# Kernel tuning notes

Measured on AMD Instinct MI355X. Metric: run time of the kernel, lower is better.

The kernel has to match this reference:

```python
import jax, jax.numpy as jnp
import numpy as np

N = 100000
E = 1600000
ROUND = 2


def spmm(src, dst, x):
    # adj.matmul(x) with binary sparse adjacency given as edge list:
    # out[dst] += x[src]
    return jax.ops.segment_sum(x[src], dst, num_segments=N)


def setup_inputs() -> dict:
    key = jax.random.key(0)
    ks = jax.random.split(key, 8)
    x = jax.random.normal(ks[0], (N, 512), dtype=jnp.float32)
    W_embed = jax.random.normal(ks[1], (512, 64), dtype=jnp.float32) * (1.0 / np.sqrt(512))
    b_embed = jnp.zeros((64,), dtype=jnp.float32)
    W_cls = jax.random.normal(ks[2], (448, 40), dtype=jnp.float32) * (1.0 / np.sqrt(448))
    b_cls = jnp.zeros((40,), dtype=jnp.float32)
    adj_src = jax.random.randint(ks[3], (E,), 0, N, dtype=jnp.int32)
    adj_dst = jax.random.randint(ks[4], (E,), 0, N, dtype=jnp.int32)
    adj2_src = jax.random.randint(ks[5], (E,), 0, N, dtype=jnp.int32)
    adj2_dst = jax.random.randint(ks[6], (E,), 0, N, dtype=jnp.int32)
    return {"x": x, "W_embed": W_embed, "b_embed": b_embed, "W_cls": W_cls,
            "b_cls": b_cls, "adj_src": adj_src, "adj_dst": adj_dst,
            "adj2_src": adj2_src, "adj2_dst": adj2_dst}


def reference(x, W_embed, b_embed, W_cls, b_cls, adj_src, adj_dst, adj2_src, adj2_dst):
    # embed: Linear + ReLU
    h = jax.nn.relu(x @ W_embed + b_embed)  # [N, 64]
    hidden_reps = [h]
    for _ in range(ROUND):
        r1 = spmm(adj_src, adj_dst, h)      # 1-hop aggregation
        r2 = spmm(adj2_src, adj2_dst, h)    # 2-hop aggregation
        h = jnp.concatenate([r1, r2], axis=-1)
        hidden_reps.append(h)
    hf = jnp.concatenate(hidden_reps, axis=-1)  # [N, 64*(2^(ROUND+1)-1)] = [N, 448]
    # dropout is identity in eval mode
    logits = hf @ W_cls + b_cls
    return jax.nn.log_softmax(logits, axis=1)
```

## Files before the change

### kernel.cpp

```cpp
#include <hip/hip_runtime.h>
#include <hip/hip_bf16.h>

#define NN 100000
#define EE 1600000
#define NBK 196
#define BSH 9
#define EPB 4096
#define NBA 391
#define STG 10240
#define CAP 9216

using frag8 = __attribute__((ext_vector_type(8))) short;
using f32x4 = __attribute__((ext_vector_type(4))) float;

__device__ inline unsigned short f2bf(float f) {
    unsigned u = __float_as_uint(f);
    u = u + 0x7FFFu + ((u >> 16) & 1u);
    return (unsigned short)(u >> 16);
}
__device__ inline unsigned pack_bf16(float a, float b) {
    __hip_bfloat162 h = __float22bfloat162_rn(float2{a, b});
    union { __hip_bfloat162 h2; unsigned u; } c;
    c.h2 = h;
    return c.u;
}
__device__ inline unsigned char f2fp8(float v) {
    unsigned p = __builtin_amdgcn_cvt_pk_fp8_f32(v, v, 0, false);
    return (unsigned char)(p & 0xff);
}


__global__ __launch_bounds__(256) void prep1_k(const int* __restrict__ s1,
                                               const int* __restrict__ d1,
                                               const int* __restrict__ s2,
                                               const int* __restrict__ d2,
                                               int* __restrict__ bcur,
                                               unsigned* __restrict__ tmp1,
                                               unsigned* __restrict__ tmp2,
                                               const float* __restrict__ W,
                                               unsigned short* __restrict__ Wbf,
                                               const float* __restrict__ Wc,
                                               unsigned short* __restrict__ Wbig) {
    __shared__ int lhist[NBK], lbase[NBK], gbase[NBK], lcur[NBK];
    __shared__ int sscan[256];
    __shared__ int stot;
    __shared__ uint2 stage[EPB];
    int blk = blockIdx.x;
    int t = threadIdx.x;

    if (blk >= 2 * NBA) {
        int wb = blk - 2 * NBA;
        if (wb < 128) {
            int id = wb * 256 + t;
            if (id < 512 * 64) {
                int k = id >> 6, col = id & 63;
                int ch = k >> 3, el = k & 7;
                int cs = (ch & ~15) | ((ch & 15) ^ (col & 7));
                Wbf[col * 512 + cs * 8 + el] = f2bf(W[id]);
            }
        } else {
            int id = (wb - 128) * 256 + t;
            int k = id >> 7, col = id & 127;
            float v = 0.f;
            if (col < 40) v = Wc[k * 40 + col];
            else if (col < 80)  { if (k >= 64) v = Wc[(192 + k - 64) * 40 + (col - 40)]; }
            else if (col < 120) { if (k >= 64) v = Wc[(320 + k - 64) * 40 + (col - 80)]; }
            int ch = k >> 3, el = k & 7;
            int phys = (ch & ~7) | ((ch & 7) ^ (col & 7));
            Wbig[col * 192 + phys * 8 + el] = f2bf(v);
        }
        return;
    }

    int adj = blk / NBA;
    int chunk = blk % NBA;
    const int* ss = adj ? s2 : s1;
    const int* dd = adj ? d2 : d1;
    unsigned* tmp = adj ? tmp2 : tmp1;
    for (int i = t; i < NBK; i += 256) { lhist[i] = 0; lcur[i] = 0; }
    __syncthreads();
    int e0 = chunk * EPB;
    int d[16], s[16];
    #pragma unroll
    for (int k = 0; k < 16; ++k) {
        int e = e0 + k * 256 + t;
        d[k] = (e < EE) ? dd[e] : -1;
        s[k] = (e < EE) ? ss[e] : 0;
        if (d[k] >= 0) atomicAdd(&lhist[d[k] >> BSH], 1);
    }
    __syncthreads();
    int hv = (t < NBK) ? lhist[t] : 0;
    sscan[t] = hv;
    __syncthreads();
    for (int off = 1; off < 256; off <<= 1) {
        int u = (t >= off) ? sscan[t - off] : 0;
        __syncthreads();
        sscan[t] += u;
        __syncthreads();
    }
    if (t < NBK) lbase[t] = sscan[t] - hv;
    if (t == NBK - 1) stot = sscan[t];
    __syncthreads();
    for (int i = t; i < NBK; i += 256)
        gbase[i] = lhist[i] ? atomicAdd(&bcur[adj * NBK + i], lhist[i]) : 0;
    __syncthreads();
    #pragma unroll
    for (int k = 0; k < 16; ++k) {
        if (d[k] >= 0) {
            int b = d[k] >> BSH;
            int pos = lbase[b] + atomicAdd(&lcur[b], 1);
            stage[pos] = make_uint2((unsigned)d[k], (unsigned)s[k]);
        }
    }
    __syncthreads();
    int tot = stot;
    for (int i = t; i < tot; i += 256) {
        uint2 u = stage[i];
        int b = u.x >> BSH;
        int off = gbase[b] + (i - lbase[b]);
        if (off < CAP)
            tmp[(size_t)b * CAP + off] = ((u.x & 511u) << 17) | u.y;
    }
}


__global__ __launch_bounds__(256) void binB_k(const unsigned* __restrict__ tmp1,
                                              const unsigned* __restrict__ tmp2,
                                              const int* __restrict__ bcur,
                                              int2* __restrict__ rse1,
                                              int2* __restrict__ rse2,
                                              int* __restrict__ csr1,
                                              int* __restrict__ csr2) {
    __shared__ int cnt[512], cur[512];
    __shared__ int sscan[256];
    __shared__ int stage[STG];
    int adj = blockIdx.y, b = blockIdx.x;
    const unsigned* tmp = adj ? tmp2 : tmp1;
    int2* rse = adj ? rse2 : rse1;
    int* csr  = adj ? csr2 : csr1;
    int t = threadIdx.x;
    int n0 = b << BSH;
    int n1 = n0 + 512; if (n1 > NN) n1 = NN;
    int nn = n1 - n0;
    int base = b * CAP;
    int count = bcur[adj * NBK + b];
    if (count > CAP) count = CAP;
    cnt[t] = 0; cnt[t + 256] = 0;
    __syncthreads();
    for (int i = t; i < count; i += 256)
        atomicAdd(&cnt[tmp[base + i] >> 17], 1);
    __syncthreads();
    int c0 = cnt[2 * t], c1 = cnt[2 * t + 1];
    int ps = c0 + c1;
    sscan[t] = ps;
    __syncthreads();
    for (int off = 1; off < 256; off <<= 1) {
        int u = (t >= off) ? sscan[t - off] : 0;
        __syncthreads();
        sscan[t] += u;
        __syncthreads();
    }
    int pe = sscan[t] - ps;
    int e0x = pe, e1x = pe + c0;
    if (2 * t < nn)     rse[n0 + 2 * t]     = make_int2(base + e0x, c0);
    if (2 * t + 1 < nn) rse[n0 + 2 * t + 1] = make_int2(base + e1x, c1);
    cur[2 * t] = e0x; cur[2 * t + 1] = e1x;
    __syncthreads();
    for (int i = t; i < count; i += 256) {
        unsigned u = tmp[base + i];
        int loc = atomicAdd(&cur[u >> 17], 1);
        int src = (int)(u & 0x1FFFFu);
        if (loc < STG) stage[loc] = src;
        else csr[base + loc] = src;
    }
    __syncthreads();
    int m = count < STG ? count : STG;
    for (int i = t; i < m; i += 256) csr[base + i] = stage[i];
}


__global__ __launch_bounds__(256) void embed_k(const float* __restrict__ x,
                                               const unsigned short* __restrict__ Wbf,
                                               const float* __restrict__ bias,
                                               unsigned short* __restrict__ hcat,
                                               unsigned char* __restrict__ h0f8) {
    __shared__ unsigned short sW[64 * 128];
    int tid = threadIdx.x;
    int lane = tid & 63, wave = tid >> 6;
    int row0 = blockIdx.x * 64;
    f32x4 acc[4];
    #pragma unroll
    for (int n = 0; n < 4; n++) acc[n] = (f32x4){0.f, 0.f, 0.f, 0.f};

    int arow = row0 + wave * 16 + (lane & 15);
    bool valid = arow < NN;
    const float* xrow = x + (size_t)(valid ? arow : 0) * 512 + (lane >> 4) * 8;

    for (int kt = 0; kt < 4; ++kt) {
        for (int q = tid; q < 1024; q += 256) {
            int col = q >> 4, c = q & 15;
            ((uint4*)sW)[q] = ((const uint4*)Wbf)[col * 64 + kt * 16 + c];
        }
        __syncthreads();
        #pragma unroll
        for (int kk = 0; kk < 4; ++kk) {
            const float4* px = (const float4*)(xrow + kt * 128 + kk * 32);
            float4 p0 = px[0], p1 = px[1];
            frag8 a;
            unsigned* au = (unsigned*)&a;
            if (valid) {
                au[0] = pack_bf16(p0.x, p0.y);
                au[1] = pack_bf16(p0.z, p0.w);
                au[2] = pack_bf16(p1.x, p1.y);
                au[3] = pack_bf16(p1.z, p1.w);
            } else {
                au[0] = 0; au[1] = 0; au[2] = 0; au[3] = 0;
            }
            #pragma unroll
            for (int n = 0; n < 4; n++) {
                int col = n * 16 + (lane & 15);
                int bc = (kk * 4 + (lane >> 4)) ^ (col & 7);
                frag8 b = *(const frag8*)&sW[(col * 16 + bc) * 8];
                acc[n] = __builtin_amdgcn_mfma_f32_16x16x32_bf16(a, b, acc[n], 0, 0, 0);
            }
        }
        __syncthreads();
    }
    #pragma unroll
    for (int n = 0; n < 4; n++) {
        int col = n * 16 + (lane & 15);
        float bv = bias[col];
        #pragma unroll
        for (int i = 0; i < 4; i++) {
            int r = row0 + wave * 16 + (lane >> 4) * 4 + i;
            if (r < NN) {
                float vv = acc[n][i] + bv;
                vv = vv > 0.f ? vv : 0.f;
                hcat[(size_t)r * 192 + col] = f2bf(vv);
                h0f8[(size_t)r * 64 + col] = f2fp8(vv);
            }
        }
    }
}


__device__ inline void gacc8f8(float* a, uint2 u) {
    a[0] += __builtin_amdgcn_cvt_f32_fp8(u.x, 0);
    a[1] += __builtin_amdgcn_cvt_f32_fp8(u.x, 1);
    a[2] += __builtin_amdgcn_cvt_f32_fp8(u.x, 2);
    a[3] += __builtin_amdgcn_cvt_f32_fp8(u.x, 3);
    a[4] += __builtin_amdgcn_cvt_f32_fp8(u.y, 0);
    a[5] += __builtin_amdgcn_cvt_f32_fp8(u.y, 1);
    a[6] += __builtin_amdgcn_cvt_f32_fp8(u.y, 2);
    a[7] += __builtin_amdgcn_cvt_f32_fp8(u.y, 3);
}


__global__ __launch_bounds__(256) void round1_k(const unsigned char* __restrict__ h8,
                                                unsigned short* __restrict__ hc,
                                                const int2* __restrict__ rse1,
                                                const int* __restrict__ csr1,
                                                const int2* __restrict__ rse2,
                                                const int* __restrict__ csr2) {
    int wave = threadIdx.x >> 6, lane = threadIdx.x & 63;
    int row = blockIdx.x * 4 + wave;
    int g = lane >> 3, gl = lane & 7;

    int2 v1r = rse1[row], v2r = rse2[row];
    int s1 = v1r.x, c1 = v1r.y, e1 = s1 + c1;
    int s2 = v2r.x, c2 = v2r.y, e2 = s2 + c2;
    int idx1 = 0, idx2 = 0;
    if (lane < c1) idx1 = csr1[s1 + lane];
    if (lane < c2) idx2 = csr2[s2 + lane];
    int cnt1 = c1 < 64 ? c1 : 64, cnt2 = c2 < 64 ? c2 : 64;

    float a1[8] = {0.f, 0.f, 0.f, 0.f, 0.f, 0.f, 0.f, 0.f};
    float a2[8] = {0.f, 0.f, 0.f, 0.f, 0.f, 0.f, 0.f, 0.f};

    {
        int j0 = g, j1 = 8 + g;
        int x10 = __shfl(idx1, j0), x11 = __shfl(idx1, j1);
        int x20 = __shfl(idx2, j0), x21 = __shfl(idx2, j1);
        uint2 u10 = *((const uint2*)(h8 + (size_t)x10 * 64) + gl);
        uint2 u11 = *((const uint2*)(h8 + (size_t)x11 * 64) + gl);
        uint2 u20 = *((const uint2*)(h8 + (size_t)x20 * 64) + gl);
        uint2 u21 = *((const uint2*)(h8 + (size_t)x21 * 64) + gl);
        if (j0 < cnt1) gacc8f8(a1, u10);
        if (j1 < cnt1) gacc8f8(a1, u11);
        if (j0 < cnt2) gacc8f8(a2, u20);
        if (j1 < cnt2) gacc8f8(a2, u21);
    }
    int nq1 = (cnt1 + 7) >> 3, nq2 = (cnt2 + 7) >> 3;
    int nq = nq1 > nq2 ? nq1 : nq2;
    for (int q = 2; q < nq; ++q) {
        int j = q * 8 + g;
        int y1 = __shfl(idx1, j), y2 = __shfl(idx2, j);
        uint2 w1 = *((const uint2*)(h8 + (size_t)y1 * 64) + gl);
        uint2 w2 = *((const uint2*)(h8 + (size_t)y2 * 64) + gl);
        if (j < cnt1) gacc8f8(a1, w1);
        if (j < cnt2) gacc8f8(a2, w2);
    }
    for (int t0 = s1 + 64; t0 < e1; t0 += 64) {
        int rem = e1 - t0;
        int idxv = 0;
        if (lane < rem) idxv = csr1[t0 + lane];
        int cnt = rem < 64 ? rem : 64;
        int nqt = (cnt + 7) >> 3;
        for (int q = 0; q < nqt; ++q) {
            int j = q * 8 + g;
            int s0 = __shfl(idxv, j);
            uint2 u = *((const uint2*)(h8 + (size_t)s0 * 64) + gl);
            if (j < cnt) gacc8f8(a1, u);
        }
    }
    for (int t0 = s2 + 64; t0 < e2; t0 += 64) {
        int rem = e2 - t0;
        int idxv = 0;
        if (lane < rem) idxv = csr2[t0 + lane];
        int cnt = rem < 64 ? rem : 64;
        int nqt = (cnt + 7) >> 3;
        for (int q = 0; q < nqt; ++q) {
            int j = q * 8 + g;
            int s0 = __shfl(idxv, j);
            uint2 u = *((const uint2*)(h8 + (size_t)s0 * 64) + gl);
            if (j < cnt) gacc8f8(a2, u);
        }
    }

    #pragma unroll
    for (int i = 0; i < 8; ++i) {
        a1[i] += __shfl_xor(a1[i], 8);
        a1[i] += __shfl_xor(a1[i], 16);
        a1[i] += __shfl_xor(a1[i], 32);
        a2[i] += __shfl_xor(a2[i], 8);
        a2[i] += __shfl_xor(a2[i], 16);
        a2[i] += __shfl_xor(a2[i], 32);
    }
    if (lane < 8) {
        uint4 o;
        o.x = pack_bf16(a1[0], a1[1]);
        o.y = pack_bf16(a1[2], a1[3]);
        o.z = pack_bf16(a1[4], a1[5]);
        o.w = pack_bf16(a1[6], a1[7]);
        *(uint4*)(hc + (size_t)row * 192 + 64 + lane * 8) = o;
    } else if (lane < 16) {
        int l = lane - 8;
        uint4 o;
        o.x = pack_bf16(a2[0], a2[1]);
        o.y = pack_bf16(a2[2], a2[3]);
        o.z = pack_bf16(a2[4], a2[5]);
        o.w = pack_bf16(a2[6], a2[7]);
        *(uint4*)(hc + (size_t)row * 192 + 128 + l * 8) = o;
    }
}


__global__ __launch_bounds__(256) void gemm_k(const unsigned short* __restrict__ hcat,
                                              const unsigned short* __restrict__ Wbig,
                                              const float* __restrict__ bc,
                                              float* __restrict__ logits,
                                              unsigned char* __restrict__ zf8) {
    __shared__ unsigned short sA[64 * 64];
    __shared__ unsigned short sB[128 * 64];
    int tid = threadIdx.x;
    int lane = tid & 63, wave = tid >> 6;
    int row0 = blockIdx.x * 64;
    f32x4 acc[8];
    #pragma unroll
    for (int n = 0; n < 8; n++) acc[n] = (f32x4){0.f, 0.f, 0.f, 0.f};

    for (int kt = 0; kt < 3; ++kt) {
        #pragma unroll
        for (int q = tid; q < 512; q += 256) {
            int r = q >> 3, c = q & 7;
            int phys = c ^ (r & 7);
            ((uint4*)sA)[r * 8 + phys] = ((const uint4*)hcat)[(size_t)(row0 + r) * 24 + kt * 8 + c];
        }
        #pragma unroll
        for (int q = tid; q < 1024; q += 256) {
            int col = q >> 3, c = q & 7;
            ((uint4*)sB)[q] = ((const uint4*)Wbig)[col * 24 + kt * 8 + c];
        }
        __syncthreads();
        #pragma unroll
        for (int kk = 0; kk < 2; ++kk) {
            int ar = wave * 16 + (lane & 15);
            int ac = (kk * 4 + (lane >> 4)) ^ (ar & 7);
            frag8 a = *(const frag8*)&sA[(ar * 8 + ac) * 8];
            #pragma unroll
            for (int n = 0; n < 8; n++) {
                int col = n * 16 + (lane & 15);
                int bcc = (kk * 4 + (lane >> 4)) ^ (col & 7);
                frag8 b = *(const frag8*)&sB[(col * 8 + bcc) * 8];
                acc[n] = __builtin_amdgcn_mfma_f32_16x16x32_bf16(a, b, acc[n], 0, 0, 0);
            }
        }
        __syncthreads();
    }
    #pragma unroll
    for (int n = 0; n < 8; n++) {
        int col = n * 16 + (lane & 15);
        float bv = (col < 40) ? bc[col] : 0.f;
        #pragma unroll
        for (int i = 0; i < 4; i++) {
            int r = row0 + wave * 16 + (lane >> 4) * 4 + i;
            if (r < NN) {
                float vv = acc[n][i];
                if (col < 40) {
                    logits[(size_t)r * 40 + col] = vv + bv;
                } else if (col < 80) {
                    zf8[(size_t)r * 128 + (col - 40)] = f2fp8(vv);
                } else if (col < 120) {
                    zf8[(size_t)r * 128 + 64 + (col - 80)] = f2fp8(vv);
                }
            }
        }
    }
}


__global__ __launch_bounds__(256) void round2_k(const unsigned char* __restrict__ z8,
                                                const int2* __restrict__ rse1,
                                                const int* __restrict__ csr1,
                                                const int2* __restrict__ rse2,
                                                const int* __restrict__ csr2,
                                                float* __restrict__ logits) {
    int wave = threadIdx.x >> 6, lane = threadIdx.x & 63;
    int row = blockIdx.x * 4 + wave;
    int g = lane >> 3, gl = lane & 7;

    int2 v1r = rse1[row], v2r = rse2[row];
    int s1 = v1r.x, c1 = v1r.y, e1 = s1 + c1;
    int s2 = v2r.x, c2 = v2r.y, e2 = s2 + c2;
    int idx1 = 0, idx2 = 0;
    if (lane < c1) idx1 = csr1[s1 + lane];
    if (lane < c2) idx2 = csr2[s2 + lane];
    int cnt1 = c1 < 64 ? c1 : 64, cnt2 = c2 < 64 ? c2 : 64;

    float a[8] = {0.f, 0.f, 0.f, 0.f, 0.f, 0.f, 0.f, 0.f};

    {
        int j0 = g, j1 = 8 + g;
        int x10 = __shfl(idx1, j0), x11 = __shfl(idx1, j1);
        int x20 = __shfl(idx2, j0), x21 = __shfl(idx2, j1);
        uint2 u10 = *((const uint2*)(z8 + (size_t)x10 * 128) + gl);
        uint2 u11 = *((const uint2*)(z8 + (size_t)x11 * 128) + gl);
        uint2 u20 = *((const uint2*)(z8 + (size_t)x20 * 128 + 64) + gl);
        uint2 u21 = *((const uint2*)(z8 + (size_t)x21 * 128 + 64) + gl);
        if (j0 < cnt1) gacc8f8(a, u10);
        if (j1 < cnt1) gacc8f8(a, u11);
        if (j0 < cnt2) gacc8f8(a, u20);
        if (j1 < cnt2) gacc8f8(a, u21);
    }
    int nq1 = (cnt1 + 7) >> 3, nq2 = (cnt2 + 7) >> 3;
    int nq = nq1 > nq2 ? nq1 : nq2;
    for (int q = 2; q < nq; ++q) {
        int j = q * 8 + g;
        int y1 = __shfl(idx1, j), y2 = __shfl(idx2, j);
        uint2 w1 = *((const uint2*)(z8 + (size_t)y1 * 128) + gl);
        uint2 w2 = *((const uint2*)(z8 + (size_t)y2 * 128 + 64) + gl);
        if (j < cnt1) gacc8f8(a, w1);
        if (j < cnt2) gacc8f8(a, w2);
    }
    for (int t0 = s1 + 64; t0 < e1; t0 += 64) {
        int rem = e1 - t0;
        int idxv = 0;
        if (lane < rem) idxv = csr1[t0 + lane];
        int cnt = rem < 64 ? rem : 64;
        int nqt = (cnt + 7) >> 3;
        for (int q = 0; q < nqt; ++q) {
            int j = q * 8 + g;
            int s0 = __shfl(idxv, j);
            uint2 u = *((const uint2*)(z8 + (size_t)s0 * 128) + gl);
            if (j < cnt) gacc8f8(a, u);
        }
    }
    for (int t0 = s2 + 64; t0 < e2; t0 += 64) {
        int rem = e2 - t0;
        int idxv = 0;
        if (lane < rem) idxv = csr2[t0 + lane];
        int cnt = rem < 64 ? rem : 64;
        int nqt = (cnt + 7) >> 3;
        for (int q = 0; q < nqt; ++q) {
            int j = q * 8 + g;
            int s0 = __shfl(idxv, j);
            uint2 u = *((const uint2*)(z8 + (size_t)s0 * 128 + 64) + gl);
            if (j < cnt) gacc8f8(a, u);
        }
    }

    #pragma unroll
    for (int i = 0; i < 8; ++i) {
        a[i] += __shfl_xor(a[i], 8);
        a[i] += __shfl_xor(a[i], 16);
        a[i] += __shfl_xor(a[i], 32);
    }

    bool act = lane < 5;
    float v[8];
    if (act) {
        float4 b0 = *(const float4*)(logits + (size_t)row * 40 + lane * 8);
        float4 b1 = *(const float4*)(logits + (size_t)row * 40 + lane * 8 + 4);
        v[0] = b0.x + a[0]; v[1] = b0.y + a[1]; v[2] = b0.z + a[2]; v[3] = b0.w + a[3];
        v[4] = b1.x + a[4]; v[5] = b1.y + a[5]; v[6] = b1.z + a[6]; v[7] = b1.w + a[7];
    } else {
        #pragma unroll
        for (int i = 0; i < 8; ++i) v[i] = -1e30f;
    }
    float m = fmaxf(fmaxf(fmaxf(v[0], v[1]), fmaxf(v[2], v[3])),
                    fmaxf(fmaxf(v[4], v[5]), fmaxf(v[6], v[7])));
    m = fmaxf(m, __shfl_xor(m, 1));
    m = fmaxf(m, __shfl_xor(m, 2));
    m = fmaxf(m, __shfl_xor(m, 4));
    float es = 0.f;
    if (act) {
        #pragma unroll
        for (int i = 0; i < 8; ++i) es += __expf(v[i] - m);
    }
    es += __shfl_xor(es, 1);
    es += __shfl_xor(es, 2);
    es += __shfl_xor(es, 4);
    float ls = __logf(es);
    if (act) {
        float4 o0, o1;
        o0.x = v[0] - m - ls; o0.y = v[1] - m - ls; o0.z = v[2] - m - ls; o0.w = v[3] - m - ls;
        o1.x = v[4] - m - ls; o1.y = v[5] - m - ls; o1.z = v[6] - m - ls; o1.w = v[7] - m - ls;
        *(float4*)(logits + (size_t)row * 40 + lane * 8)     = o0;
        *(float4*)(logits + (size_t)row * 40 + lane * 8 + 4) = o1;
    }
}


extern "C" void kernel_launch(void* const* d_in, const int* in_sizes, int n_in,
                              void* d_out, int out_size, void* d_ws, size_t ws_size,
                              hipStream_t stream) {
    const float* x       = (const float*)d_in[0];
    const float* W_embed = (const float*)d_in[1];
    const float* b_embed = (const float*)d_in[2];
    const float* W_cls   = (const float*)d_in[3];
    const float* b_cls   = (const float*)d_in[4];
    const int* a1src = (const int*)d_in[5];
    const int* a1dst = (const int*)d_in[6];
    const int* a2src = (const int*)d_in[7];
    const int* a2dst = (const int*)d_in[8];

    float* logits = (float*)d_out;
    float* ws = (float*)d_ws;

    const size_t OFF_HCAT = 0;
    const size_t OFF_H0F8 = 9600000;
    const size_t OFF_ZF8  = 11200000;
    const size_t OFF_RSE1 = 14400000;
    const size_t OFF_RSE2 = 14600000;
    const size_t OFF_BC   = 14800000;
    const size_t OFF_CSR1 = 14800392;
    const size_t OFF_CSR2 = 16606728;
    const size_t OFF_TMP1 = 18413064;
    const size_t OFF_TMP2 = 20219400;
    const size_t OFF_WBF  = 22025736;
    const size_t OFF_WBIG = 22042120;

    unsigned short* hcat = (unsigned short*)(ws + OFF_HCAT);
    unsigned char*  h0f8 = (unsigned char*)(ws + OFF_H0F8);
    unsigned char*  zf8  = (unsigned char*)(ws + OFF_ZF8);
    int2* rse1 = (int2*)(ws + OFF_RSE1);
    int2* rse2 = (int2*)(ws + OFF_RSE2);
    int*  bcur = (int*)(ws + OFF_BC);
    int*  csr1 = (int*)(ws + OFF_CSR1);
    int*  csr2 = (int*)(ws + OFF_CSR2);
    unsigned* tmp1 = (unsigned*)(ws + OFF_TMP1);
    unsigned* tmp2 = (unsigned*)(ws + OFF_TMP2);
    unsigned short* wbf  = (unsigned short*)(ws + OFF_WBF);
    unsigned short* wbig = (unsigned short*)(ws + OFF_WBIG);

    hipMemsetAsync(ws + OFF_BC, 0, 392 * 4, stream);

    prep1_k<<<2 * NBA + 224, 256, 0, stream>>>(a1src, a1dst, a2src, a2dst, bcur, tmp1, tmp2,
                                               W_embed, wbf, W_cls, wbig);
    binB_k<<<dim3(NBK, 2), 256, 0, stream>>>(tmp1, tmp2, bcur, rse1, rse2, csr1, csr2);

    embed_k<<<(NN + 63) / 64, 256, 0, stream>>>(x, wbf, b_embed, hcat, h0f8);

    round1_k<<<NN / 4, 256, 0, stream>>>(h0f8, hcat, rse1, csr1, rse2, csr2);
    gemm_k<<<(NN + 63) / 64, 256, 0, stream>>>(hcat, wbig, b_cls, logits, zf8);
    round2_k<<<NN / 4, 256, 0, stream>>>(zf8, rse1, csr1, rse2, csr2, logits);
}
```

Baseline: 251.0 us.

## Fuse CSR binning and embed GEMM into one heterogeneous kernel launch

After: 249.6 us. Within noise of the previous version (-0.6%).

```diff
diff --git a/kernel.cpp b/kernel.cpp
--- a/kernel.cpp
+++ b/kernel.cpp
@@ -7,7 +7,7 @@
 #define BSH 9
 #define EPB 4096
 #define NBA 391
-#define STG 10240
+#define STG 8704
 #define CAP 9216
 
 using frag8 = __attribute__((ext_vector_type(8))) short;
@@ -124,70 +124,74 @@
 }
 
 
-__global__ __launch_bounds__(256) void binB_k(const unsigned* __restrict__ tmp1,
-                                              const unsigned* __restrict__ tmp2,
-                                              const int* __restrict__ bcur,
-                                              int2* __restrict__ rse1,
-                                              int2* __restrict__ rse2,
-                                              int* __restrict__ csr1,
-                                              int* __restrict__ csr2) {
-    __shared__ int cnt[512], cur[512];
-    __shared__ int sscan[256];
-    __shared__ int stage[STG];
-    int adj = blockIdx.y, b = blockIdx.x;
-    const unsigned* tmp = adj ? tmp2 : tmp1;
-    int2* rse = adj ? rse2 : rse1;
-    int* csr  = adj ? csr2 : csr1;
-    int t = threadIdx.x;
-    int n0 = b << BSH;
-    int n1 = n0 + 512; if (n1 > NN) n1 = NN;
-    int nn = n1 - n0;
-    int base = b * CAP;
-    int count = bcur[adj * NBK + b];
-    if (count > CAP) count = CAP;
-    cnt[t] = 0; cnt[t + 256] = 0;
-    __syncthreads();
-    for (int i = t; i < count; i += 256)
-        atomicAdd(&cnt[tmp[base + i] >> 17], 1);
-    __syncthreads();
-    int c0 = cnt[2 * t], c1 = cnt[2 * t + 1];
-    int ps = c0 + c1;
-    sscan[t] = ps;
-    __syncthreads();
-    for (int off = 1; off < 256; off <<= 1) {
-        int u = (t >= off) ? sscan[t - off] : 0;
-        __syncthreads();
-        sscan[t] += u;
-        __syncthreads();
-    }
-    int pe = sscan[t] - ps;
-    int e0x = pe, e1x = pe + c0;
-    if (2 * t < nn)     rse[n0 + 2 * t]     = make_int2(base + e0x, c0);
-    if (2 * t + 1 < nn) rse[n0 + 2 * t + 1] = make_int2(base + e1x, c1);
-    cur[2 * t] = e0x; cur[2 * t + 1] = e1x;
-    __syncthreads();
-    for (int i = t; i < count; i += 256) {
-        unsigned u = tmp[base + i];
-        int loc = atomicAdd(&cur[u >> 17], 1);
-        int src = (int)(u & 0x1FFFFu);
-        if (loc < STG) stage[loc] = src;
-        else csr[base + loc] = src;
-    }
-    __syncthreads();
-    int m = count < STG ? count : STG;
-    for (int i = t; i < m; i += 256) csr[base + i] = stage[i];
-}
-
-
-__global__ __launch_bounds__(256) void embed_k(const float* __restrict__ x,
+__global__ __launch_bounds__(256) void prep2_k(const unsigned* __restrict__ tmp1,
+                                               const unsigned* __restrict__ tmp2,
+                                               const int* __restrict__ bcur,
+                                               int2* __restrict__ rse1,
+                                               int2* __restrict__ rse2,
+                                               int* __restrict__ csr1,
+                                               int* __restrict__ csr2,
+                                               const float* __restrict__ x,
                                                const unsigned short* __restrict__ Wbf,
                                                const float* __restrict__ bias,
                                                unsigned short* __restrict__ hcat,
                                                unsigned char* __restrict__ h0f8) {
-    __shared__ unsigned short sW[64 * 128];
-    int tid = threadIdx.x;
-    int lane = tid & 63, wave = tid >> 6;
-    int row0 = blockIdx.x * 64;
+    __shared__ __align__(16) unsigned char smem[(512 + 512 + 256 + STG) * 4];
+    int blk = blockIdx.x;
+    int t = threadIdx.x;
+
+    if (blk < 2 * NBK) {
+        int* cnt   = (int*)smem;
+        int* cur   = cnt + 512;
+        int* sscan = cur + 512;
+        int* stage = sscan + 256;
+        int adj = blk / NBK, b = blk % NBK;
+        const unsigned* tmp = adj ? tmp2 : tmp1;
+        int2* rse = adj ? rse2 : rse1;
+        int* csr  = adj ? csr2 : csr1;
+        int n0 = b << BSH;
+        int n1 = n0 + 512; if (n1 > NN) n1 = NN;
+        int nn = n1 - n0;
+        int base = b * CAP;
+        int count = bcur[adj * NBK + b];
+        if (count > CAP) count = CAP;
+        cnt[t] = 0; cnt[t + 256] = 0;
+        __syncthreads();
+        for (int i = t; i < count; i += 256)
+            atomicAdd(&cnt[tmp[base + i] >> 17], 1);
+        __syncthreads();
+        int c0 = cnt[2 * t], c1 = cnt[2 * t + 1];
+        int ps = c0 + c1;
+        sscan[t] = ps;
+        __syncthreads();
+        for (int off = 1; off < 256; off <<= 1) {
+            int u = (t >= off) ? sscan[t - off] : 0;
+            __syncthreads();
+            sscan[t] += u;
+            __syncthreads();
+        }
+        int pe = sscan[t] - ps;
+        int e0x = pe, e1x = pe + c0;
+        if (2 * t < nn)     rse[n0 + 2 * t]     = make_int2(base + e0x, c0);
+        if (2 * t + 1 < nn) rse[n0 + 2 * t + 1] = make_int2(base + e1x, c1);
+        cur[2 * t] = e0x; cur[2 * t + 1] = e1x;
+        __syncthreads();
+        for (int i = t; i < count; i += 256) {
+            unsigned u = tmp[base + i];
+            int loc = atomicAdd(&cur[u >> 17], 1);
+            int src = (int)(u & 0x1FFFFu);
+            if (loc < STG) stage[loc] = src;
+            else csr[base + loc] = src;
+        }
+        __syncthreads();
+        int m = count < STG ? count : STG;
+        for (int i = t; i < m; i += 256) csr[base + i] = stage[i];
+        return;
+    }
+
+    unsigned short* sW = (unsigned short*)smem;
+    int lane = t & 63, wave = t >> 6;
+    int row0 = (blk - 2 * NBK) * 64;
     f32x4 acc[4];
     #pragma unroll
     for (int n = 0; n < 4; n++) acc[n] = (f32x4){0.f, 0.f, 0.f, 0.f};
@@ -197,7 +201,7 @@
     const float* xrow = x + (size_t)(valid ? arow : 0) * 512 + (lane >> 4) * 8;
 
     for (int kt = 0; kt < 4; ++kt) {
-        for (int q = tid; q < 1024; q += 256) {
+        for (int q = t; q < 1024; q += 256) {
             int col = q >> 4, c = q & 15;
             ((uint4*)sW)[q] = ((const uint4*)Wbf)[col * 64 + kt * 16 + c];
         }
@@ -577,9 +581,9 @@
 
     prep1_k<<<2 * NBA + 224, 256, 0, stream>>>(a1src, a1dst, a2src, a2dst, bcur, tmp1, tmp2,
                                                W_embed, wbf, W_cls, wbig);
-    binB_k<<<dim3(NBK, 2), 256, 0, stream>>>(tmp1, tmp2, bcur, rse1, rse2, csr1, csr2);
-
-    embed_k<<<(NN + 63) / 64, 256, 0, stream>>>(x, wbf, b_embed, hcat, h0f8);
+    prep2_k<<<2 * NBK + (NN + 63) / 64, 256, 0, stream>>>(tmp1, tmp2, bcur,
+                                                          rse1, rse2, csr1, csr2,
+                                                          x, wbf, b_embed, hcat, h0f8);
 
     round1_k<<<NN / 4, 256, 0, stream>>>(h0f8, hcat, rse1, csr1, rse2, csr2);
     gemm_k<<<(NN + 63) / 64, 256, 0, stream>>>(hcat, wbig, b_cls, logits, zf8);
```
